# Kernel tuning notes

Hardware: AMD Instinct MI355X
Metric: run time of the kernel (lower is better)

The kernel has to match this reference:

```python
import jax, jax.numpy as jnp
import numpy as np

N = 100000       # nodes
E = 1600000      # edges (avg degree 16)
D = 8            # node feat dim per layer (feat_dims=[8,8,8])
SE = 2           # static edge feats
EF = SE + 1 + D  # static + euclidian norm + direction vector = 11
NLAYERS = 2
EPS_BN = 1e-5
EPS_NORM = 1e-12
LRELU_SLOPE = 0.01


def setup_inputs() -> dict:
    key = jax.random.key(0)
    ks = jax.random.split(key, 3 + 6 * NLAYERS)
    inp = {
        "v": jax.random.normal(ks[0], (N, D), jnp.float32),
        "edge_index": jax.random.randint(ks[1], (2, E), 0, N, dtype=jnp.int64),
        "edge_attr": jax.random.uniform(ks[2], (E, SE), jnp.float32),
    }
    for l in range(NLAYERS):
        kk = ks[3 + 6 * l: 3 + 6 * (l + 1)]
        inp[f"en_w{l}"] = jax.random.normal(kk[0], (EF, D * D), jnp.float32) * 0.1
        inp[f"en_b{l}"] = jnp.zeros((D * D,), jnp.float32)
        inp[f"en_g{l}"] = jnp.ones((D * D,), jnp.float32)
        inp[f"en_beta{l}"] = jnp.zeros((D * D,), jnp.float32)
        inp[f"root_w{l}"] = jax.random.normal(kk[1], (D, D), jnp.float32) * 0.1
        inp[f"root_b{l}"] = jnp.zeros((D,), jnp.float32)
    return inp


def _edge_feat(vres, edge_attr, src, dst):
    # gather endpoints, L2-normalize difference, concat [static | norm | direction]
    d = vres[dst] - vres[src]                       # [E, D]
    n = jnp.linalg.norm(d, axis=1, keepdims=True)   # [E, 1]
    dirv = d / (n + EPS_NORM)                       # [E, D]
    return jnp.concatenate([edge_attr[:, :SE], n, dirv], axis=1)  # [E, EF]


def _gnn_layer(x, e, src, dst, en_w, en_b, en_g, en_beta, root_w, root_b):
    # edge_net: Linear -> BatchNorm1d (training stats) -> Tanh
    h = e @ en_w + en_b                             # [E, D*D]
    mu = jnp.mean(h, axis=0)
    var = jnp.var(h, axis=0)
    h = (h - mu) * jax.lax.rsqrt(var + EPS_BN) * en_g + en_beta
    w = jnp.tanh(h).reshape(-1, D, D)               # [E, D, D]
    # gather-matmul-scatter (NNConv-style, mean aggregation at dst)
    msg = jnp.einsum('ei,eio->eo', x[src], w)       # [E, D]
    agg = jax.ops.segment_sum(msg, dst, num_segments=N)
    cnt = jax.ops.segment_sum(jnp.ones((msg.shape[0], 1), msg.dtype), dst,
                              num_segments=N)
    agg = agg / jnp.maximum(cnt, 1.0)
    out = agg + x @ root_w + root_b                 # root_weight=True
    return jax.nn.leaky_relu(out, LRELU_SLOPE)      # act=True


def reference(v, edge_index, edge_attr,
              en_w0, en_b0, en_g0, en_beta0, root_w0, root_b0,
              en_w1, en_b1, en_g1, en_beta1, root_w1, root_b1):
    src, dst = edge_index[0], edge_index[1]
    vres = v
    layer_params = [
        (en_w0, en_b0, en_g0, en_beta0, root_w0, root_b0),
        (en_w1, en_b1, en_g1, en_beta1, root_w1, root_b1),
    ]
    for p in layer_params:  # dynamic_efeats='skip': edge feats from vres each layer
        e = _edge_feat(vres, edge_attr, src, dst)
        v = _gnn_layer(v, e, src, dst, *p)
    return v + vres  # residual=True
```

## Files before the change

kernel.cpp:

```cpp
#include <hip/hip_runtime.h>
#include <hip/hip_fp16.h>
#include <math.h>

#define NN 100000
#define NE 1600000
#define EPS_BN 1e-5f
#define EPS_NORM 1e-12f
#define SLOPE 0.01f
#define NBUCK 391
#define NBLK 391
#define EPB 4096
#define CNT_LEN (NBUCK * NBLK)
#define CSB ((CNT_LEN + 255) / 256)
#define GS_LEN (64 * NBUCK)
#define GS_BLOCKS ((GS_LEN + 255) / 256)
#define MAXB 6144

typedef _Float16 h2 __attribute__((ext_vector_type(2)));

#if __has_builtin(__builtin_amdgcn_exp2f)
#define EXP2F(x) __builtin_amdgcn_exp2f(x)
#else
#define EXP2F(x) exp2f(x)
#endif

__device__ __forceinline__ float fast_tanh(float x) {
    float t = EXP2F(x * 2.885390082f);
    return fmaf(-2.0f, __builtin_amdgcn_rcpf(t + 1.0f), 1.0f);
}

__device__ __forceinline__ unsigned pk2(float a, float b) {
    union { __half2 h; unsigned u; } c;
    c.h = __float22half2_rn(make_float2(a, b));
    return c.u;
}

#if __has_builtin(__builtin_amdgcn_fdot2)
__device__ __forceinline__ float fdot2u(unsigned a, unsigned b, float c) {
    union { unsigned u; h2 h; } ca, cb;
    ca.u = a; cb.u = b;
    return __builtin_amdgcn_fdot2(ca.h, cb.h, c, false);
}
#else
__device__ __forceinline__ float fdot2u(unsigned a, unsigned b, float c) {
    float d;
    asm("v_dot2_f32_f16 %0, %1, %2, %3" : "=v"(d) : "v"(a), "v"(b), "v"(c));
    return d;
}
#endif

__global__ void __launch_bounds__(256) r1_count_kernel(
    const int* __restrict__ ei, int* __restrict__ cntT)
{
    __shared__ int h[NBUCK];
    int b = blockIdx.x, t = threadIdx.x;
    for (int j = t; j < NBUCK; j += 256) h[j] = 0;
    __syncthreads();
#pragma unroll
    for (int it = 0; it < 4; ++it) {
        int e4 = b * EPB + it * 1024 + t * 4;
        if (e4 < NE) {
            int4 d4 = *(const int4*)(ei + NE + e4);
            atomicAdd(&h[d4.x >> 8], 1);
            atomicAdd(&h[d4.y >> 8], 1);
            atomicAdd(&h[d4.z >> 8], 1);
            atomicAdd(&h[d4.w >> 8], 1);
        }
    }
    __syncthreads();
    for (int j = t; j < NBUCK; j += 256) cntT[(size_t)j * NBLK + b] = h[j];
}

__global__ void __launch_bounds__(256) gscanA_kernel(
    int* __restrict__ a, int* __restrict__ bs, int len)
{
    int b = blockIdx.x, t = threadIdx.x;
    int i = b * 256 + t;
    int d = (i < len) ? a[i] : 0;
    __shared__ int sh[256];
    sh[t] = d;
    __syncthreads();
    for (int off = 1; off < 256; off <<= 1) {
        int val = (t >= off) ? sh[t - off] : 0;
        __syncthreads();
        sh[t] += val;
        __syncthreads();
    }
    if (i < len) a[i] = sh[t] - d;
    if (t == 255) bs[b] = sh[255];
}

__global__ void __launch_bounds__(256) gscanB_kernel(
    int* __restrict__ a, const int* __restrict__ bs, int len)
{
    int b = blockIdx.x, t = threadIdx.x;
    __shared__ int sh[256];
    int s = 0;
    for (int j = t; j < b; j += 256) s += bs[j];
    sh[t] = s;
    __syncthreads();
    for (int off = 128; off > 0; off >>= 1) {
        if (t < off) sh[t] += sh[t + off];
        __syncthreads();
    }
    int boff = sh[0];
    int i = b * 256 + t;
    if (i < len) a[i] += boff;
}

__global__ void __launch_bounds__(256) r2_scatter_kernel(
    const int* __restrict__ ei, const float* __restrict__ ea,
    const int* __restrict__ cntT, unsigned long long* __restrict__ bucketed)
{
    __shared__ int h[NBUCK];
    __shared__ int base[NBUCK];
    int b = blockIdx.x, t = threadIdx.x;
    for (int j = t; j < NBUCK; j += 256) {
        h[j] = 0;
        base[j] = cntT[(size_t)j * NBLK + b];
    }
    __syncthreads();
#pragma unroll
    for (int it = 0; it < 4; ++it) {
        int e4 = b * EPB + it * 1024 + t * 4;
        if (e4 < NE) {
            int4 s4 = *(const int4*)(ei + e4);
            int4 d4 = *(const int4*)(ei + NE + e4);
            float4 a01 = *(const float4*)(ea + 2 * (size_t)e4);
            float4 a23 = *(const float4*)(ea + 2 * (size_t)e4 + 4);
#define DO_EDGE(S, D, A0, A1)                                                \
            {                                                                \
                unsigned a0q = __float2uint_rn((A0) * 32768.0f);             \
                if (a0q > 32767u) a0q = 32767u;                              \
                unsigned a1q = __float2uint_rn((A1) * 32768.0f);             \
                if (a1q > 32767u) a1q = 32767u;                              \
                unsigned long long rec =                                     \
                      (((unsigned long long)(unsigned)(D)) << 47)            \
                    | (((unsigned long long)(unsigned)(S)) << 30)            \
                    | (((unsigned long long)a0q) << 15)                      \
                    | ((unsigned long long)a1q);                             \
                int bb = (D) >> 8;                                           \
                int lr = atomicAdd(&h[bb], 1);                               \
                bucketed[base[bb] + lr] = rec;                               \
            }
            DO_EDGE(s4.x, d4.x, a01.x, a01.y)
            DO_EDGE(s4.y, d4.y, a01.z, a01.w)
            DO_EDGE(s4.z, d4.z, a23.x, a23.y)
            DO_EDGE(s4.w, d4.w, a23.z, a23.w)
#undef DO_EDGE
        }
    }
}

__global__ void __launch_bounds__(512)
__attribute__((amdgpu_waves_per_eu(2, 4))) finalize_kernel(
    const unsigned long long* __restrict__ bucketed,
    const int* __restrict__ cntT,
    const float* __restrict__ v,
    uint4* __restrict__ A16, uint2* __restrict__ B8,
    int* __restrict__ rowptr, int* __restrict__ pr, int* __restrict__ bhT,
    float* __restrict__ partials)
{
    __shared__ int hist[256], lps[256], lh[64];
    __shared__ unsigned short pos16[MAXB];
    __shared__ unsigned char dl8[MAXB];
    __shared__ unsigned short inv16[MAXB];
    __shared__ float lsum[8][77];
    int b = blockIdx.x, t = threadIdx.x;
    if (t < 256) hist[t] = 0;
    if (t < 64) lh[t] = 0;
    __syncthreads();
    int bstart = cntT[(size_t)b * NBLK];
    int bend = (b == NBUCK - 1) ? NE : cntT[(size_t)(b + 1) * NBLK];
    int bsize = bend - bstart;

    for (int o = t; o < bsize; o += 512) {
        unsigned long long r = bucketed[bstart + o];
        int dl = (int)((r >> 47) & 255u);
        int lr = atomicAdd(&hist[dl], 1);
        pos16[o] = (unsigned short)lr;
        dl8[o] = (unsigned char)dl;
    }
    __syncthreads();
    int d = (t < 256) ? hist[t] : 0;
    if (t < 256) lps[t] = d;
    __syncthreads();
    for (int off = 1; off < 256; off <<= 1) {
        int val = (t >= off && t < 256) ? lps[t - off] : 0;
        __syncthreads();
        if (t < 256) lps[t] += val;
        __syncthreads();
    }
    int node = b * 256 + t;
    if (t < 256 && node < NN) {
        rowptr[node] = bstart + lps[t] - d;
        int db = d < 63 ? d : 63;
        int bkt = 63 - db;
        int lr2 = atomicAdd(&lh[bkt], 1);
        pr[node] = (lr2 << 6) | bkt;
    }
    if (b == 0 && t == 0) rowptr[NN] = NE;
    __syncthreads();
    if (t < 64) bhT[t * NBUCK + b] = lh[t];

    for (int o = t; o < bsize; o += 512) {
        int dl = (int)dl8[o];
        int fp = (lps[dl] - hist[dl]) + (int)pos16[o];
        inv16[fp] = (unsigned short)o;
    }
    __syncthreads();

    float acc[39];
#pragma unroll
    for (int i = 0; i < 39; ++i) acc[i] = 0.0f;

    for (int p = t; (p - (t & 1)) < bsize; p += 512) {
        bool valid = p < bsize;
        float e[11];
        if (valid) {
            int o = (int)inv16[p];
            unsigned long long r = bucketed[bstart + o];
            int dl = (int)((r >> 47) & 255u);
            int s = (int)((r >> 30) & 0x1FFFFu);
            float a0 = (float)(unsigned)((r >> 15) & 0x7FFFu) * (1.0f / 32768.0f);
            float a1 = (float)(unsigned)(r & 0x7FFFu) * (1.0f / 32768.0f);
            int dn = b * 256 + dl;
            float4 s0 = *(const float4*)(v + (size_t)s * 8);
            float4 s1 = *(const float4*)(v + (size_t)s * 8 + 4);
            float4 d0 = *(const float4*)(v + (size_t)dn * 8);
            float4 d1 = *(const float4*)(v + (size_t)dn * 8 + 4);
            float df[8];
            df[0] = d0.x - s0.x; df[1] = d0.y - s0.y;
            df[2] = d0.z - s0.z; df[3] = d0.w - s0.w;
            df[4] = d1.x - s1.x; df[5] = d1.y - s1.y;
            df[6] = d1.z - s1.z; df[7] = d1.w - s1.w;
            float nsq = 0.0f;
#pragma unroll
            for (int q = 0; q < 8; ++q) nsq = fmaf(df[q], df[q], nsq);
            float nrm = sqrtf(nsq);
            float inv = __builtin_amdgcn_rcpf(nrm + EPS_NORM);
            e[0] = a0; e[1] = a1; e[2] = nrm;
#pragma unroll
            for (int q = 0; q < 8; ++q) e[3 + q] = df[q] * inv;

            uint4 lo;
            lo.x = pk2(e[0], e[1]); lo.y = pk2(e[2], e[3]);
            lo.z = pk2(e[4], e[5]); lo.w = pk2(e[6], e[7]);
            A16[bstart + p] = lo;
            unsigned q10 = __float2uint_rn((e[10] + 1.0f) * 16383.5f);
            if (q10 > 32767u) q10 = 32767u;
            uint2 hv;
            hv.x = pk2(e[8], e[9]);
            hv.y = ((unsigned)s << 15) | q10;
            B8[bstart + p] = hv;
        } else {
#pragma unroll
            for (int k = 0; k < 11; ++k) e[k] = 0.0f;
        }
        float eo[11];
#pragma unroll
        for (int k = 0; k < 11; ++k) eo[k] = __shfl_xor(e[k], 1);
        if (!(t & 1)) {
#pragma unroll
            for (int k = 0; k < 11; ++k) acc[k] += e[k] + eo[k];
            int p2 = 11;
#pragma unroll
            for (int k = 0; k < 11; ++k)
#pragma unroll
                for (int l = k; l < 11; ++l) {
                    if (p2 < 39) {
                        acc[p2] = fmaf(e[k], e[l], acc[p2]);
                        acc[p2] = fmaf(eo[k], eo[l], acc[p2]);
                    }
                    ++p2;
                }
        } else {
            int p2 = 11;
#pragma unroll
            for (int k = 0; k < 11; ++k)
#pragma unroll
                for (int l = k; l < 11; ++l) {
                    if (p2 >= 39) {
                        acc[p2 - 39] = fmaf(e[k], e[l], acc[p2 - 39]);
                        acc[p2 - 39] = fmaf(eo[k], eo[l], acc[p2 - 39]);
                    }
                    ++p2;
                }
        }
    }

#pragma unroll
    for (int i = 0; i < 39; ++i) {
        float x = acc[i];
        x += __shfl_down(x, 2);
        x += __shfl_down(x, 4);
        x += __shfl_down(x, 8);
        x += __shfl_down(x, 16);
        x += __shfl_down(x, 32);
        acc[i] = x;
    }
    int wave = t >> 6;
    int lane = t & 63;
    if (lane == 0) {
#pragma unroll
        for (int i = 0; i < 39; ++i) lsum[wave][i] = acc[i];
    }
    if (lane == 1) {
#pragma unroll
        for (int i = 0; i < 38; ++i) lsum[wave][39 + i] = acc[i];
    }
    __syncthreads();
    if (t < 77) {
        float s = 0.0f;
#pragma unroll
        for (int w = 0; w < 8; ++w) s += lsum[w][t];
        partials[b * 77 + t] = s;
    }
}

__global__ void bn_finalize_kernel(
    const float* __restrict__ partials,
    const float* __restrict__ w0, const float* __restrict__ b0,
    const float* __restrict__ g0, const float* __restrict__ be0,
    const float* __restrict__ w1, const float* __restrict__ b1,
    const float* __restrict__ g1, const float* __restrict__ be1,
    float* __restrict__ wbp)
{
    __shared__ double gs[77];
    int t = threadIdx.x;
    if (t < 77) {
        double s = 0.0;
        for (int b = 0; b < NBUCK; ++b) s += (double)partials[b * 77 + t];
        gs[t] = s;
    }
    __syncthreads();
    if (t >= 128) return;
    int layer = t >> 6;
    int c = t & 63;
    const float* W  = layer ? w1 : w0;
    const float* B  = layer ? b1 : b0;
    const float* G  = layer ? g1 : g0;
    const float* BE = layer ? be1 : be0;

    const double invE = 1.0 / (double)NE;
    double m[11], wv[11];
    for (int k = 0; k < 11; ++k) {
        m[k] = gs[k] * invE;
        wv[k] = (double)W[k * 64 + c];
    }
    double md = 0.0;
    for (int k = 0; k < 11; ++k) md += m[k] * wv[k];
    double s2 = 0.0;
    int p = 11;
    for (int k = 0; k < 11; ++k)
        for (int l = k; l < 11; ++l) {
            double Me = gs[p] * invE; ++p;
            double term = Me * wv[k] * wv[l];
            s2 += (k == l) ? term : 2.0 * term;
        }
    double var = s2 - md * md;
    double mu = md + (double)B[c];
    float scale = (float)((double)G[c] / sqrt(var + (double)EPS_BN));
    float shift = (float)((double)BE[c] - mu * (double)scale);

    float* wpd = wbp + layer * 1152;
    for (int k = 0; k < 11; ++k) wpd[k * 64 + c] = W[k * 64 + c] * scale;
    wpd[704 + c] = fmaf(B[c], scale, shift);
    unsigned* pw = (unsigned*)(wpd + 768);
    for (int kp = 0; kp < 5; ++kp) {
        float wlo = W[(2 * kp) * 64 + c] * scale;
        float whi = W[(2 * kp + 1) * 64 + c] * scale;
        pw[kp * 64 + c] = pk2(wlo, whi);
    }
}

__global__ void __launch_bounds__(256) permB_kernel(
    const int* __restrict__ pr, const int* __restrict__ bhT,
    const int* __restrict__ rowptr, int4* __restrict__ perm4)
{
    int n = blockIdx.x * 256 + threadIdx.x;
    if (n >= NN) return;
    int p = pr[n];
    int bkt = p & 63, lrank = p >> 6, b = n >> 8;
    int pos = bhT[bkt * NBUCK + b] + lrank;
    perm4[pos] = make_int4(n, rowptr[n], rowptr[n + 1], 0);
}

#define FAT_BODY3(LO, HB, E10, XI)                                           \
    do {                                                                     \
        _Pragma("unroll")                                                    \
        for (int o = 0; o < 8; ++o) {                                        \
            float hh = breg[o];                                              \
            hh = fdot2u((LO).x, pw[0][o], hh);                               \
            hh = fdot2u((LO).y, pw[1][o], hh);                               \
            hh = fdot2u((LO).z, pw[2][o], hh);                               \
            hh = fdot2u((LO).w, pw[3][o], hh);                               \
            hh = fdot2u((HB).x, pw[4][o], hh);                               \
            hh = fmaf((E10), w10[o], hh);                                    \
            msg[o] = fmaf((XI), fast_tanh(hh), msg[o]);                      \
        }                                                                    \
    } while (0)

template<int LAYER>
__global__ void __launch_bounds__(256)
__attribute__((amdgpu_waves_per_eu(2, 6))) layer_fat_kernel(
    const float* __restrict__ vres,
    const float* __restrict__ x,
    const uint4* __restrict__ A16, const uint2* __restrict__ B8,
    const int4* __restrict__ perm4,
    const float* __restrict__ wb,
    const float* __restrict__ rw, const float* __restrict__ rb,
    float* __restrict__ out)
{
    int g = blockIdx.x * 256 + threadIdx.x;
    int4 pm = perm4[g >> 3];
    int n = pm.x, rp0 = pm.y, rp1 = pm.z;
    int i = g & 7;

    unsigned pw[5][8];
    const unsigned* pwg = (const unsigned*)(wb + 768);
#pragma unroll
    for (int kp = 0; kp < 5; ++kp) {
        uint4 pa = *(const uint4*)(pwg + kp * 64 + i * 8);
        uint4 pb = *(const uint4*)(pwg + kp * 64 + i * 8 + 4);
        pw[kp][0] = pa.x; pw[kp][1] = pa.y; pw[kp][2] = pa.z; pw[kp][3] = pa.w;
        pw[kp][4] = pb.x; pw[kp][5] = pb.y; pw[kp][6] = pb.z; pw[kp][7] = pb.w;
    }
    float w10[8];
    {
        float4 wa = *(const float4*)(wb + 640 + i * 8);
        float4 wc = *(const float4*)(wb + 640 + i * 8 + 4);
        w10[0] = wa.x; w10[1] = wa.y; w10[2] = wa.z; w10[3] = wa.w;
        w10[4] = wc.x; w10[5] = wc.y; w10[6] = wc.z; w10[7] = wc.w;
    }
    float breg[8];
    {
        float4 ba = *(const float4*)(wb + 704 + i * 8);
        float4 bb = *(const float4*)(wb + 704 + i * 8 + 4);
        breg[0] = ba.x; breg[1] = ba.y; breg[2] = ba.z; breg[3] = ba.w;
        breg[4] = bb.x; breg[5] = bb.y; breg[6] = bb.z; breg[7] = bb.w;
    }

    float4 vd0 = *(const float4*)(vres + (size_t)n * 8);
    float4 vd1 = *(const float4*)(vres + (size_t)n * 8 + 4);
    float vd[8] = {vd0.x, vd0.y, vd0.z, vd0.w, vd1.x, vd1.y, vd1.z, vd1.w};

    float msg[8];
#pragma unroll
    for (int o = 0; o < 8; ++o) msg[o] = 0.0f;

    int j = rp0;
    for (; j + 2 <= rp1; j += 2) {
        uint4 lo0 = A16[j];
        uint4 lo1 = A16[j + 1];
        uint2 hb0 = B8[j];
        uint2 hb1 = B8[j + 1];
        int s0 = (int)(hb0.y >> 15);
        int s1 = (int)(hb1.y >> 15);
        float e10a = fmaf((float)(hb0.y & 0x7FFFu), 1.0f / 16383.5f, -1.0f);
        float e10b = fmaf((float)(hb1.y & 0x7FFFu), 1.0f / 16383.5f, -1.0f);
        float xi0 = x[(size_t)s0 * 8 + i];
        float xi1 = x[(size_t)s1 * 8 + i];
        FAT_BODY3(lo0, hb0, e10a, xi0);
        FAT_BODY3(lo1, hb1, e10b, xi1);
    }
    if (j < rp1) {
        uint4 lo0 = A16[j];
        uint2 hb0 = B8[j];
        int s0 = (int)(hb0.y >> 15);
        float e10a = fmaf((float)(hb0.y & 0x7FFFu), 1.0f / 16383.5f, -1.0f);
        float xi0 = x[(size_t)s0 * 8 + i];
        FAT_BODY3(lo0, hb0, e10a, xi0);
    }

#pragma unroll
    for (int o = 0; o < 8; ++o) {
        float m = msg[o];
        m += __shfl_xor(m, 1);
        m += __shfl_xor(m, 2);
        m += __shfl_xor(m, 4);
        msg[o] = m;
    }
    float mo = msg[0];
#pragma unroll
    for (int o = 1; o < 8; ++o) if (i == o) mo = msg[o];

    float cf = (float)(rp1 - rp0);
    float invc = __builtin_amdgcn_rcpf(fmaxf(cf, 1.0f));

    float xn[8];
    if (LAYER == 0) {
#pragma unroll
        for (int q = 0; q < 8; ++q) xn[q] = vd[q];
    } else {
        float4 x0 = *(const float4*)(x + (size_t)n * 8);
        float4 x1 = *(const float4*)(x + (size_t)n * 8 + 4);
        xn[0] = x0.x; xn[1] = x0.y; xn[2] = x0.z; xn[3] = x0.w;
        xn[4] = x1.x; xn[5] = x1.y; xn[6] = x1.z; xn[7] = x1.w;
    }
    float a = fmaf(mo, invc, rb[i]);
#pragma unroll
    for (int k = 0; k < 8; ++k) a = fmaf(xn[k], rw[k * 8 + i], a);
    float y = (a > 0.0f) ? a : SLOPE * a;
    if (LAYER == 1) y += vres[(size_t)n * 8 + i];
    out[(size_t)n * 8 + i] = y;
}

extern "C" void kernel_launch(void* const* d_in, const int* in_sizes, int n_in,
                              void* d_out, int out_size, void* d_ws, size_t ws_size,
                              hipStream_t stream) {
    const float* v  = (const float*)d_in[0];
    const int* ei   = (const int*)d_in[1];
    const float* ea = (const float*)d_in[2];
    const float* en_w0  = (const float*)d_in[3];
    const float* en_b0  = (const float*)d_in[4];
    const float* en_g0  = (const float*)d_in[5];
    const float* en_be0 = (const float*)d_in[6];
    const float* rw0    = (const float*)d_in[7];
    const float* rb0    = (const float*)d_in[8];
    const float* en_w1  = (const float*)d_in[9];
    const float* en_b1  = (const float*)d_in[10];
    const float* en_g1  = (const float*)d_in[11];
    const float* en_be1 = (const float*)d_in[12];
    const float* rw1    = (const float*)d_in[13];
    const float* rb1    = (const float*)d_in[14];

    char* ws = (char*)d_ws;
    float* partials = (float*)(ws);
    float* wbp      = (float*)(ws + 131072);
    int*   rowptr   = (int*)  (ws + 143360);
    int*   pr       = (int*)  (ws + 543744);
    int4*  perm4    = (int4*) (ws + 944128);
    int*   bhT      = (int*)  (ws + 2544128);
    int*   gbsum    = (int*)  (ws + 2644224);
    int*   cbsum    = (int*)  (ws + 2644736);
    int*   cntT     = (int*)  (ws + 2648064);
    float* v1       = (float*)(ws + 3259904);
    unsigned long long* bucketed = (unsigned long long*)(ws + 6460416);
    uint4* A16      = (uint4*)(ws + 19260416);
    uint2* B8       = (uint2*)(ws + 44860416);
    float* vout     = (float*)d_out;

    r1_count_kernel<<<NBLK, 256, 0, stream>>>(ei, cntT);
    gscanA_kernel<<<CSB, 256, 0, stream>>>(cntT, cbsum, CNT_LEN);
    gscanB_kernel<<<CSB, 256, 0, stream>>>(cntT, cbsum, CNT_LEN);
    r2_scatter_kernel<<<NBLK, 256, 0, stream>>>(ei, ea, cntT, bucketed);
    finalize_kernel<<<NBUCK, 512, 0, stream>>>(bucketed, cntT, v, A16, B8,
                                               rowptr, pr, bhT, partials);
    gscanA_kernel<<<GS_BLOCKS, 256, 0, stream>>>(bhT, gbsum, GS_LEN);
    gscanB_kernel<<<GS_BLOCKS, 256, 0, stream>>>(bhT, gbsum, GS_LEN);
    permB_kernel<<<NBUCK, 256, 0, stream>>>(pr, bhT, rowptr, perm4);
    bn_finalize_kernel<<<1, 128, 0, stream>>>(partials, en_w0, en_b0, en_g0, en_be0,
                                              en_w1, en_b1, en_g1, en_be1, wbp);

    const int LB = (NN * 8) / 256;
    layer_fat_kernel<0><<<LB, 256, 0, stream>>>(v, v,  A16, B8, perm4, wbp,        rw0, rb0, v1);
    layer_fat_kernel<1><<<LB, 256, 0, stream>>>(v, v1, A16, B8, perm4, wbp + 1152, rw1, rb1, vout);
}
```

Measured before the change: 201.7 us.

## Split per-node layer work across 32 lanes, two output columns each

Each destination node is now handled by 32 threads instead of 8, with each thread computing two of the eight output columns for its input row. This shrinks the per-thread weight register footprint and the per-edge compute chain, which should raise occupancy and latency hiding. The cost is four times as many threads, each reloading the same edge records and source features, plus redundant epilogue work where only one lane in eight writes.

After: 248.5 us. +23.2%, slower.

```diff
diff --git a/kernel.cpp b/kernel.cpp
--- a/kernel.cpp
+++ b/kernel.cpp
@@ -386,24 +386,21 @@
     perm4[pos] = make_int4(n, rowptr[n], rowptr[n + 1], 0);
 }
 
-#define FAT_BODY3(LO, HB, E10, XI)                                           \
+#define EDGE32(LO, HB, E10, XI)                                              \
     do {                                                                     \
-        _Pragma("unroll")                                                    \
-        for (int o = 0; o < 8; ++o) {                                        \
-            float hh = breg[o];                                              \
-            hh = fdot2u((LO).x, pw[0][o], hh);                               \
-            hh = fdot2u((LO).y, pw[1][o], hh);                               \
-            hh = fdot2u((LO).z, pw[2][o], hh);                               \
-            hh = fdot2u((LO).w, pw[3][o], hh);                               \
-            hh = fdot2u((HB).x, pw[4][o], hh);                               \
-            hh = fmaf((E10), w10[o], hh);                                    \
-            msg[o] = fmaf((XI), fast_tanh(hh), msg[o]);                      \
-        }                                                                    \
+        float h0 = br.x, h1 = br.y;                                          \
+        h0 = fdot2u((LO).x, pw0.x, h0); h1 = fdot2u((LO).x, pw0.y, h1);      \
+        h0 = fdot2u((LO).y, pw1.x, h0); h1 = fdot2u((LO).y, pw1.y, h1);      \
+        h0 = fdot2u((LO).z, pw2.x, h0); h1 = fdot2u((LO).z, pw2.y, h1);      \
+        h0 = fdot2u((LO).w, pw3.x, h0); h1 = fdot2u((LO).w, pw3.y, h1);      \
+        h0 = fdot2u((HB).x, pw4.x, h0); h1 = fdot2u((HB).x, pw4.y, h1);      \
+        h0 = fmaf((E10), w10.x, h0);    h1 = fmaf((E10), w10.y, h1);         \
+        m0 = fmaf((XI), fast_tanh(h0), m0);                                  \
+        m1 = fmaf((XI), fast_tanh(h1), m1);                                  \
     } while (0)
 
 template<int LAYER>
-__global__ void __launch_bounds__(256)
-__attribute__((amdgpu_waves_per_eu(2, 6))) layer_fat_kernel(
+__global__ void __launch_bounds__(256) layer_fat_kernel(
     const float* __restrict__ vres,
     const float* __restrict__ x,
     const uint4* __restrict__ A16, const uint2* __restrict__ B8,
@@ -413,41 +410,23 @@
     float* __restrict__ out)
 {
     int g = blockIdx.x * 256 + threadIdx.x;
-    int4 pm = perm4[g >> 3];
+    int4 pm = perm4[g >> 5];
     int n = pm.x, rp0 = pm.y, rp1 = pm.z;
-    int i = g & 7;
-
-    unsigned pw[5][8];
+    int l5 = g & 31;
+    int i = l5 & 7;
+    int o0 = (l5 >> 3) * 2;
+    int c = i * 8 + o0;
+
     const unsigned* pwg = (const unsigned*)(wb + 768);
-#pragma unroll
-    for (int kp = 0; kp < 5; ++kp) {
-        uint4 pa = *(const uint4*)(pwg + kp * 64 + i * 8);
-        uint4 pb = *(const uint4*)(pwg + kp * 64 + i * 8 + 4);
-        pw[kp][0] = pa.x; pw[kp][1] = pa.y; pw[kp][2] = pa.z; pw[kp][3] = pa.w;
-        pw[kp][4] = pb.x; pw[kp][5] = pb.y; pw[kp][6] = pb.z; pw[kp][7] = pb.w;
-    }
-    float w10[8];
-    {
-        float4 wa = *(const float4*)(wb + 640 + i * 8);
-        float4 wc = *(const float4*)(wb + 640 + i * 8 + 4);
-        w10[0] = wa.x; w10[1] = wa.y; w10[2] = wa.z; w10[3] = wa.w;
-        w10[4] = wc.x; w10[5] = wc.y; w10[6] = wc.z; w10[7] = wc.w;
-    }
-    float breg[8];
-    {
-        float4 ba = *(const float4*)(wb + 704 + i * 8);
-        float4 bb = *(const float4*)(wb + 704 + i * 8 + 4);
-        breg[0] = ba.x; breg[1] = ba.y; breg[2] = ba.z; breg[3] = ba.w;
-        breg[4] = bb.x; breg[5] = bb.y; breg[6] = bb.z; breg[7] = bb.w;
-    }
-
-    float4 vd0 = *(const float4*)(vres + (size_t)n * 8);
-    float4 vd1 = *(const float4*)(vres + (size_t)n * 8 + 4);
-    float vd[8] = {vd0.x, vd0.y, vd0.z, vd0.w, vd1.x, vd1.y, vd1.z, vd1.w};
-
-    float msg[8];
-#pragma unroll
-    for (int o = 0; o < 8; ++o) msg[o] = 0.0f;
+    uint2 pw0 = *(const uint2*)(pwg + 0 * 64 + c);
+    uint2 pw1 = *(const uint2*)(pwg + 1 * 64 + c);
+    uint2 pw2 = *(const uint2*)(pwg + 2 * 64 + c);
+    uint2 pw3 = *(const uint2*)(pwg + 3 * 64 + c);
+    uint2 pw4 = *(const uint2*)(pwg + 4 * 64 + c);
+    float2 w10 = *(const float2*)(wb + 640 + c);
+    float2 br  = *(const float2*)(wb + 704 + c);
+
+    float m0 = 0.0f, m1 = 0.0f;
 
     int j = rp0;
     for (; j + 2 <= rp1; j += 2) {
@@ -461,8 +440,8 @@
         float e10b = fmaf((float)(hb1.y & 0x7FFFu), 1.0f / 16383.5f, -1.0f);
         float xi0 = x[(size_t)s0 * 8 + i];
         float xi1 = x[(size_t)s1 * 8 + i];
-        FAT_BODY3(lo0, hb0, e10a, xi0);
-        FAT_BODY3(lo1, hb1, e10b, xi1);
+        EDGE32(lo0, hb0, e10a, xi0);
+        EDGE32(lo1, hb1, e10b, xi1);
     }
     if (j < rp1) {
         uint4 lo0 = A16[j];
@@ -470,40 +449,37 @@
         int s0 = (int)(hb0.y >> 15);
         float e10a = fmaf((float)(hb0.y & 0x7FFFu), 1.0f / 16383.5f, -1.0f);
         float xi0 = x[(size_t)s0 * 8 + i];
-        FAT_BODY3(lo0, hb0, e10a, xi0);
-    }
-
-#pragma unroll
-    for (int o = 0; o < 8; ++o) {
-        float m = msg[o];
-        m += __shfl_xor(m, 1);
-        m += __shfl_xor(m, 2);
-        m += __shfl_xor(m, 4);
-        msg[o] = m;
-    }
-    float mo = msg[0];
-#pragma unroll
-    for (int o = 1; o < 8; ++o) if (i == o) mo = msg[o];
+        EDGE32(lo0, hb0, e10a, xi0);
+    }
+
+    m0 += __shfl_xor(m0, 1); m1 += __shfl_xor(m1, 1);
+    m0 += __shfl_xor(m0, 2); m1 += __shfl_xor(m1, 2);
+    m0 += __shfl_xor(m0, 4); m1 += __shfl_xor(m1, 4);
 
     float cf = (float)(rp1 - rp0);
     float invc = __builtin_amdgcn_rcpf(fmaxf(cf, 1.0f));
 
-    float xn[8];
-    if (LAYER == 0) {
-#pragma unroll
-        for (int q = 0; q < 8; ++q) xn[q] = vd[q];
-    } else {
-        float4 x0 = *(const float4*)(x + (size_t)n * 8);
-        float4 x1 = *(const float4*)(x + (size_t)n * 8 + 4);
-        xn[0] = x0.x; xn[1] = x0.y; xn[2] = x0.z; xn[3] = x0.w;
-        xn[4] = x1.x; xn[5] = x1.y; xn[6] = x1.z; xn[7] = x1.w;
-    }
-    float a = fmaf(mo, invc, rb[i]);
-#pragma unroll
-    for (int k = 0; k < 8; ++k) a = fmaf(xn[k], rw[k * 8 + i], a);
-    float y = (a > 0.0f) ? a : SLOPE * a;
-    if (LAYER == 1) y += vres[(size_t)n * 8 + i];
-    out[(size_t)n * 8 + i] = y;
+    float4 x0 = *(const float4*)(x + (size_t)n * 8);
+    float4 x1 = *(const float4*)(x + (size_t)n * 8 + 4);
+    float xn[8] = {x0.x, x0.y, x0.z, x0.w, x1.x, x1.y, x1.z, x1.w};
+
+    float a0 = fmaf(m0, invc, rb[o0]);
+    float a1 = fmaf(m1, invc, rb[o0 + 1]);
+#pragma unroll
+    for (int k = 0; k < 8; ++k) {
+        a0 = fmaf(xn[k], rw[k * 8 + o0], a0);
+        a1 = fmaf(xn[k], rw[k * 8 + o0 + 1], a1);
+    }
+    float y0 = (a0 > 0.0f) ? a0 : SLOPE * a0;
+    float y1 = (a1 > 0.0f) ? a1 : SLOPE * a1;
+    if (LAYER == 1) {
+        y0 += vres[(size_t)n * 8 + o0];
+        y1 += vres[(size_t)n * 8 + o0 + 1];
+    }
+    if (i == 0) {
+        out[(size_t)n * 8 + o0] = y0;
+        out[(size_t)n * 8 + o0 + 1] = y1;
+    }
 }
 
 extern "C" void kernel_launch(void* const* d_in, const int* in_sizes, int n_in,
@@ -553,7 +529,7 @@
     bn_finalize_kernel<<<1, 128, 0, stream>>>(partials, en_w0, en_b0, en_g0, en_be0,
                                               en_w1, en_b1, en_g1, en_be1, wbp);
 
-    const int LB = (NN * 8) / 256;
-    layer_fat_kernel<0><<<LB, 256, 0, stream>>>(v, v,  A16, B8, perm4, wbp,        rw0, rb0, v1);
-    layer_fat_kernel<1><<<LB, 256, 0, stream>>>(v, v1, A16, B8, perm4, wbp + 1152, rw1, rb1, vout);
-}
+    const int LB32 = (NN * 32) / 256;
+    layer_fat_kernel<0><<<LB32, 256, 0, stream>>>(v, v,  A16, B8, perm4, wbp,        rw0, rb0, v1);
+    layer_fat_kernel<1><<<LB32, 256, 0, stream>>>(v, v1, A16, B8, perm4, wbp + 1152, rw1, rb1, vout);
+}
```
